# Performance work log

Measured on AMD Instinct MI355X. Metric: run time of the kernel, lower is better.

Reference implementation:

```python
import jax, jax.numpy as jnp
import numpy as np

N = 100000
E = 500000
HID = 256
N_EDGE_TYPES = 5
N_ATOM = 16
N_CHARGE = 7
NUM_RBF = 16
CUTOFF = 5.0
LN_EPS = 1e-5


def _xavier(key, shape):
    fan_in, fan_out = shape[0], shape[1]
    lim = float(np.sqrt(6.0 / (fan_in + fan_out)))
    return jax.random.uniform(key, shape, jnp.float32, -lim, lim)


def setup_inputs() -> dict:
    key = jax.random.key(0)
    ks = jax.random.split(key, 12)
    input_dim = HID * 2 + NUM_RBF + N_ATOM + N_CHARGE  # 551
    h = jax.random.normal(ks[0], (N, HID), jnp.float32)
    x = jax.random.normal(ks[1], (N, 3), jnp.float32)
    spawn_node_idx = jax.random.randint(ks[2], (E,), 0, N)
    existing_node_idx = jax.random.randint(ks[3], (E,), 0, N)
    ins_x = jax.random.normal(ks[4], (E, 3), jnp.float32)
    ins_a = jax.random.randint(ks[5], (E,), 0, N_ATOM)
    ins_c = jax.random.randint(ks[6], (E,), 0, N_CHARGE)
    # MLP params (Xavier weights, zero biases; LayerNorm gamma=1, beta=0)
    W1 = _xavier(ks[7], (input_dim, HID)); b1 = jnp.zeros((HID,), jnp.float32)
    g1 = jnp.ones((HID,), jnp.float32); be1 = jnp.zeros((HID,), jnp.float32)
    W2 = _xavier(ks[8], (HID, HID // 2)); b2 = jnp.zeros((HID // 2,), jnp.float32)
    g2 = jnp.ones((HID // 2,), jnp.float32); be2 = jnp.zeros((HID // 2,), jnp.float32)
    W3 = _xavier(ks[9], (HID // 2, N_EDGE_TYPES)); b3 = jnp.zeros((N_EDGE_TYPES,), jnp.float32)
    # Gaussian RBF parameters: centers on [0, cutoff], shared width from spacing
    rbf_mu = jnp.linspace(0.0, CUTOFF, NUM_RBF).astype(jnp.float32)
    delta = CUTOFF / (NUM_RBF - 1)
    rbf_gamma = jnp.asarray(1.0 / (2.0 * delta * delta), jnp.float32)
    return {"h": h, "x": x, "spawn_node_idx": spawn_node_idx,
            "existing_node_idx": existing_node_idx, "ins_x": ins_x,
            "ins_a": ins_a, "ins_c": ins_c,
            "W1": W1, "b1": b1, "g1": g1, "be1": be1,
            "W2": W2, "b2": b2, "g2": g2, "be2": be2,
            "W3": W3, "b3": b3, "rbf_mu": rbf_mu, "rbf_gamma": rbf_gamma}


def _layer_norm(z, gamma, beta):
    mu = jnp.mean(z, axis=-1, keepdims=True)
    var = jnp.mean((z - mu) ** 2, axis=-1, keepdims=True)
    return (z - mu) * jax.lax.rsqrt(var + LN_EPS) * gamma + beta


def reference(h, x, spawn_node_idx, existing_node_idx, ins_x, ins_a, ins_c,
              W1, b1, g1, be1, W2, b2, g2, be2, W3, b3, rbf_mu, rbf_gamma):
    # gather node pairs  [E, HID] / [E, 3]
    h_spawn = h[spawn_node_idx]
    h_existing = h[existing_node_idx]
    existing_pos = x[existing_node_idx]
    # distance + Gaussian RBF  [E, NUM_RBF]
    d = jnp.maximum(jnp.linalg.norm(ins_x - existing_pos, axis=-1), 1e-6)
    dist_features = jnp.exp(-rbf_gamma * (d[:, None] - rbf_mu) ** 2)
    # one-hot insertion type features
    ins_atom = jax.nn.one_hot(ins_a, N_ATOM, dtype=h.dtype)
    ins_charge = jax.nn.one_hot(ins_c, N_CHARGE, dtype=h.dtype)
    feats = jnp.concatenate([h_spawn, h_existing, dist_features, ins_atom, ins_charge], axis=-1)
    # 3-layer MLP: Linear -> LN -> SiLU -> Linear -> LN -> SiLU -> Linear
    z = jax.nn.silu(_layer_norm(feats @ W1 + b1, g1, be1))
    z = jax.nn.silu(_layer_norm(z @ W2 + b2, g2, be2))
    return z @ W3 + b3  # [E, N_EDGE_TYPES]
```

## Files before the change

kernel.cpp:

```cpp
#include <hip/hip_runtime.h>
#include <stdint.h>

#define NN 100000
#define EE 500000
#define HIDD 256
#define LN_EPS 1e-5f

typedef _Float16 half8 __attribute__((ext_vector_type(8)));
typedef _Float16 half4 __attribute__((ext_vector_type(4)));
typedef __fp16 fp16x2 __attribute__((ext_vector_type(2)));
typedef float f32x4 __attribute__((ext_vector_type(4)));
typedef float f32x2 __attribute__((ext_vector_type(2)));

#define LBAR() asm volatile("s_waitcnt lgkmcnt(0)\n\ts_barrier" ::: "memory")

__device__ __forceinline__ unsigned short f2h(float f) {
  _Float16 h = (_Float16)f;
  union { _Float16 hh; unsigned short us; } u; u.hh = h;
  return u.us;
}

__device__ __forceinline__ unsigned pkrtz(float a, float b) {
  union { fp16x2 h; unsigned u; } c;
  c.h = __builtin_amdgcn_cvt_pkrtz(a, b);
  return c.u;
}

__device__ __forceinline__ float fast_silu(float y) {
  float e = __expf(-y);
  return y * __builtin_amdgcn_rcpf(1.f + e);
}

__device__ __forceinline__ half8 ldg8(const unsigned short* p) {
  return *(const half8*)p;
}

__device__ __forceinline__ int4 cvt_row(const float* s) {
  float4 a0 = *(const float4*)s, a1 = *(const float4*)(s + 4);
  uint4 ua;
  ua.x = pkrtz(a0.x, a0.y); ua.y = pkrtz(a0.z, a0.w);
  ua.z = pkrtz(a1.x, a1.y); ua.w = pkrtz(a1.z, a1.w);
  return *(int4*)&ua;
}

__global__ __launch_bounds__(256) void prep_kern(const float* __restrict__ h,
                                                 const float* __restrict__ W1,
                                                 const float* __restrict__ W2,
                                                 const float* __restrict__ W3,
                                                 unsigned short* __restrict__ hb,
                                                 unsigned short* __restrict__ w1sw,
                                                 unsigned short* __restrict__ w2sw,
                                                 unsigned short* __restrict__ w3sw) {
  int b = blockIdx.x;
  if (b < 712) {
    int t = b * 256 + threadIdx.x;
    if (t < 147456) {
      int chunk = t >> 14, rem = t & 16383;
      int kq = rem >> 11, n = (rem >> 3) & 255, j = rem & 7;
      int k = (chunk << 6) + (kq << 3) + j;
      float v = (k < 551) ? W1[k * 256 + n] : 0.f;
      w1sw[t] = f2h(v);
    } else if (t < 147456 + 32768) {
      int t2 = t - 147456;
      int chunk = t2 >> 13, rem = t2 & 8191;
      int kq = rem >> 10, n = (rem >> 3) & 127, j = rem & 7;
      int k = (chunk << 6) + (kq << 3) + j;
      w2sw[t2] = f2h(W2[k * 128 + n]);
    } else if (t < 147456 + 32768 + 2048) {
      int t3 = t - 180224;
      int kq = t3 >> 7, o = (t3 >> 3) & 15, j = t3 & 7;
      int k = (kq << 3) + j;
      w3sw[t3] = f2h((o < 5) ? W3[k * 5 + o] : 0.f);
    }
  } else {
    int i = ((b - 712) * 256 + threadIdx.x) * 8;
    float4 v0 = *(const float4*)(h + i);
    float4 v1 = *(const float4*)(h + i + 4);
    uint4 u;
    u.x = pkrtz(v0.x, v0.y); u.y = pkrtz(v0.z, v0.w);
    u.z = pkrtz(v1.x, v1.y); u.w = pkrtz(v1.z, v1.w);
    *(uint4*)(hb + i) = u;
  }
}

struct __align__(16) SMem {
  short r1[16384];
  float red[512];
  _Float16 b1h[256], g1h[256], be1h[256];
  _Float16 b2h[128], g2h[128], be2h[128];
  float muv[16];
  float b3v[8];
  int spI[64], exI[64];
};

__global__ __launch_bounds__(256, 3)
void edge_head_main(const float* __restrict__ h, const float* __restrict__ x,
                    const int* __restrict__ spawn, const int* __restrict__ exist,
                    const float* __restrict__ insx, const int* __restrict__ insa,
                    const int* __restrict__ insc,
                    const float* __restrict__ b1, const float* __restrict__ g1,
                    const float* __restrict__ be1,
                    const float* __restrict__ b2, const float* __restrict__ g2,
                    const float* __restrict__ be2,
                    const float* __restrict__ b3, const float* __restrict__ mu,
                    const float* __restrict__ gammaP,
                    const unsigned short* __restrict__ w1sw,
                    const unsigned short* __restrict__ w2sw,
                    const unsigned short* __restrict__ w3swg,
                    const unsigned short* __restrict__ hb, int use_hb,
                    float* __restrict__ out) {
  __shared__ SMem sm;
  const int t = threadIdx.x;
  const int base = blockIdx.x * 64;
  const int lane = t & 63;
  const int wv = t >> 6;
  const int cl = lane & 15;
  const int q = lane >> 4;
  const int sx = (cl & 7) << 3;

  sm.b1h[t] = (_Float16)b1[t]; sm.g1h[t] = (_Float16)g1[t]; sm.be1h[t] = (_Float16)be1[t];
  if (t < 128) { sm.b2h[t] = (_Float16)b2[t]; sm.g2h[t] = (_Float16)g2[t]; sm.be2h[t] = (_Float16)be2[t]; }
  if (t < 16) sm.muv[t] = mu[t];
  if (t < 8) sm.b3v[t] = (t < 5) ? b3[t] : 0.f;
  if (t < 64) {
    int e = base + t; int ec = e < EE ? e : EE - 1;
    sm.spI[t] = spawn[ec]; sm.exI[t] = exist[ec];
  }
  const float gma = gammaP[0];

  LBAR();

  float dreg = 0.f;
  int k1 = 16, k2 = 32;
  if (t < 64) {
    int e = base + t; int ec = e < EE ? e : EE - 1;
    float ix0 = insx[ec * 3], ix1 = insx[ec * 3 + 1], ix2 = insx[ec * 3 + 2];
    int nd = sm.exI[t];
    float dx = ix0 - x[nd * 3], dy = ix1 - x[nd * 3 + 1], dz = ix2 - x[nd * 3 + 2];
    dreg = fmaxf(sqrtf(dx * dx + dy * dy + dz * dz), 1e-6f);
    k1 = 16 + insa[ec]; k2 = 32 + insc[ec];
  }

  const int row0 = t >> 3, p0 = t & 7;
  const int row1 = row0 + 32;
  const int sw0 = ((p0 ^ (row0 & 7)) << 3);
  const int sw1 = ((p0 ^ (row1 & 7)) << 3);

  const size_t oSp0 = (size_t)sm.spI[row0] * HIDD + p0 * 8;
  const size_t oSp1 = (size_t)sm.spI[row1] * HIDD + p0 * 8;
  const size_t oEx0 = (size_t)sm.exI[row0] * HIDD + p0 * 8;
  const size_t oEx1 = (size_t)sm.exI[row1] * HIDD + p0 * 8;
  const char* bSp0 = use_hb ? (const char*)(hb + oSp0) : (const char*)(h + oSp0);
  const char* bSp1 = use_hb ? (const char*)(hb + oSp1) : (const char*)(h + oSp1);
  const char* bEx0 = use_hb ? (const char*)(hb + oEx0) : (const char*)(h + oEx0);
  const char* bEx1 = use_hb ? (const char*)(hb + oEx1) : (const char*)(h + oEx1);

#define GLOAD(lc, PA, PB) do {                                          \
    const int g_ = (lc) - 1;                                            \
    const int colb_ = (g_ & 3) * 64;                                    \
    const char* b0_ = (g_ < 4) ? bSp0 : bEx0;                           \
    const char* b1_ = (g_ < 4) ? bSp1 : bEx1;                           \
    if (use_hb) {                                                       \
      PA = *(const int4*)(b0_ + colb_ * 2);                             \
      PB = *(const int4*)(b1_ + colb_ * 2);                             \
    } else {                                                            \
      PA = cvt_row((const float*)(b0_ + colb_ * 4));                    \
      PB = cvt_row((const float*)(b1_ + colb_ * 4));                    \
    }                                                                   \
  } while (0)

  int4 pA1, pB1, pA0, pB0;
  GLOAD(1, pA1, pB1);
  GLOAD(2, pA0, pB0);

  const unsigned short* w1p = w1sw + q * 2048 + wv * 512 + cl * 8;
  half8 fA[4], fB[4];
#pragma unroll
  for (int i = 0; i < 4; ++i) fA[i] = ldg8(w1p + 8 * 16384 + i * 128);
#pragma unroll
  for (int i = 0; i < 4; ++i) fB[i] = ldg8(w1p + 8 * 16384 + 8192 + i * 128);

  if (t < 64) {
    short* rp = &sm.r1[t * 64];
    const int sw = t & 7;
    float rb[16];
#pragma unroll
    for (int k = 0; k < 16; ++k) { float dd = dreg - sm.muv[k]; rb[k] = __expf(-gma * dd * dd); }
    uint4 ua, ub;
    ua.x = pkrtz(rb[0], rb[1]);  ua.y = pkrtz(rb[2], rb[3]);
    ua.z = pkrtz(rb[4], rb[5]);  ua.w = pkrtz(rb[6], rb[7]);
    ub.x = pkrtz(rb[8], rb[9]);  ub.y = pkrtz(rb[10], rb[11]);
    ub.z = pkrtz(rb[12], rb[13]); ub.w = pkrtz(rb[14], rb[15]);
    *(int4*)&rp[(0 ^ sw) * 8] = *(int4*)&ua;
    *(int4*)&rp[(1 ^ sw) * 8] = *(int4*)&ub;
    const int4 z4 = {0, 0, 0, 0};
#pragma unroll
    for (int g = 2; g < 8; ++g) *(int4*)&rp[(g ^ sw) * 8] = z4;
    rp[((k1 >> 3) ^ sw) * 8 + (k1 & 7)] = (short)0x3C00;
    rp[((k2 >> 3) ^ sw) * 8 + (k2 & 7)] = (short)0x3C00;
  }

  LBAR();

  f32x4 acc[4][4];
#pragma unroll
  for (int i = 0; i < 4; ++i)
#pragma unroll
    for (int j = 0; j < 4; ++j) acc[i][j] = (f32x4){0.f, 0.f, 0.f, 0.f};

#pragma unroll
  for (int c = 0; c < 9; ++c) {
    if (c < 8) {
      const int nb = ((c + 1) & 1) * 4096;
      if ((c & 1) == 0) {
        *(int4*)&sm.r1[nb + row0 * 64 + sw0] = pA1;
        *(int4*)&sm.r1[nb + row1 * 64 + sw1] = pB1;
        if (c <= 5) GLOAD(c + 3, pA1, pB1);
      } else {
        *(int4*)&sm.r1[nb + row0 * 64 + sw0] = pA0;
        *(int4*)&sm.r1[nb + row1 * 64 + sw1] = pB0;
        if (c <= 5) GLOAD(c + 3, pA0, pB0);
      }
    }
    const int cb = (c & 1) * 4096;
    {
      half8 bf[4];
#pragma unroll
      for (int j = 0; j < 4; ++j)
        bf[j] = *(const half8*)&sm.r1[cb + (j * 16 + cl) * 64 + ((q * 8) ^ sx)];
#pragma unroll
      for (int i = 0; i < 4; ++i)
#pragma unroll
        for (int j = 0; j < 4; ++j)
          acc[i][j] = __builtin_amdgcn_mfma_f32_16x16x32_f16(fA[i], bf[j], acc[i][j], 0, 0, 0);
    }
    if (c < 8) {
      const unsigned short* wp = w1p + c * 16384;
#pragma unroll
      for (int i = 0; i < 4; ++i) fA[i] = ldg8(wp + i * 128);
    }
    {
      half8 bf[4];
#pragma unroll
      for (int j = 0; j < 4; ++j)
        bf[j] = *(const half8*)&sm.r1[cb + (j * 16 + cl) * 64 + ((32 + q * 8) ^ sx)];
#pragma unroll
      for (int i = 0; i < 4; ++i)
#pragma unroll
        for (int j = 0; j < 4; ++j)
          acc[i][j] = __builtin_amdgcn_mfma_f32_16x16x32_f16(fB[i], bf[j], acc[i][j], 0, 0, 0);
    }
    if (c < 8) {
      const unsigned short* wp = w1p + c * 16384 + 8192;
#pragma unroll
      for (int i = 0; i < 4; ++i) fB[i] = ldg8(wp + i * 128);
    }
    LBAR();
  }
#undef GLOAD

  f32x2 bb1[4][2];
#pragma unroll
  for (int i = 0; i < 4; ++i) {
    half4 b4 = *(const half4*)&sm.b1h[wv * 64 + i * 16 + q * 4];
    bb1[i][0] = (f32x2){(float)b4[0], (float)b4[1]};
    bb1[i][1] = (f32x2){(float)b4[2], (float)b4[3]};
  }
  float S1arr[4], Q1arr[4];
#pragma unroll
  for (int j = 0; j < 4; ++j) {
    f32x2 S2 = (f32x2){0.f, 0.f}, Q2 = (f32x2){0.f, 0.f};
#pragma unroll
    for (int i = 0; i < 4; ++i) {
      f32x2 v0 = (f32x2){acc[i][j][0], acc[i][j][1]} + bb1[i][0];
      f32x2 v1 = (f32x2){acc[i][j][2], acc[i][j][3]} + bb1[i][1];
      acc[i][j][0] = v0[0]; acc[i][j][1] = v0[1];
      acc[i][j][2] = v1[0]; acc[i][j][3] = v1[1];
      S2 += v0 + v1;
      Q2 += v0 * v0;
      Q2 += v1 * v1;
    }
    float S = S2[0] + S2[1], Q = Q2[0] + Q2[1];
    S += __shfl_xor(S, 16); S += __shfl_xor(S, 32);
    Q += __shfl_xor(Q, 16); Q += __shfl_xor(Q, 32);
    S1arr[j] = S; Q1arr[j] = Q;
  }
  if (q == 0) {
#pragma unroll
    for (int j = 0; j < 4; ++j) {
      sm.red[wv * 64 + j * 16 + cl] = S1arr[j];
      sm.red[256 + wv * 64 + j * 16 + cl] = Q1arr[j];
    }
  }
  LBAR();
  f32x2 rs1[4], mr1[4];
#pragma unroll
  for (int j = 0; j < 4; ++j) {
    int m = j * 16 + cl;
    float S = sm.red[m] + sm.red[64 + m] + sm.red[128 + m] + sm.red[192 + m];
    float Q = sm.red[256 + m] + sm.red[320 + m] + sm.red[384 + m] + sm.red[448 + m];
    float mn = S * (1.f / 256.f);
    float rs = rsqrtf(Q * (1.f / 256.f) - mn * mn + LN_EPS);
    rs1[j] = (f32x2){rs, rs};
    mr1[j] = (f32x2){-mn * rs, -mn * rs};
  }
#pragma unroll
  for (int i = 0; i < 4; ++i) {
    half4 g4 = *(const half4*)&sm.g1h[wv * 64 + i * 16 + q * 4];
    half4 e4 = *(const half4*)&sm.be1h[wv * 64 + i * 16 + q * 4];
    f32x2 gg0 = (f32x2){(float)g4[0], (float)g4[1]}, gg1 = (f32x2){(float)g4[2], (float)g4[3]};
    f32x2 ee0 = (f32x2){(float)e4[0], (float)e4[1]}, ee1 = (f32x2){(float)e4[2], (float)e4[3]};
#pragma unroll
    for (int j = 0; j < 4; ++j) {
      f32x2 v0 = (f32x2){acc[i][j][0], acc[i][j][1]};
      f32x2 v1 = (f32x2){acc[i][j][2], acc[i][j][3]};
      f32x2 t0 = v0 * rs1[j] + mr1[j];
      f32x2 t1 = v1 * rs1[j] + mr1[j];
      f32x2 y0 = t0 * gg0 + ee0;
      f32x2 y1 = t1 * gg1 + ee1;
      float s0 = fast_silu(y0[0]), s1 = fast_silu(y0[1]);
      float s2 = fast_silu(y1[0]), s3 = fast_silu(y1[1]);
      uint2 w; w.x = pkrtz(s0, s1); w.y = pkrtz(s2, s3);
      int m = j * 16 + cl;
      int k0 = wv * 64 + i * 16 + q * 4;
      *(uint2*)&sm.r1[m * 256 + (k0 ^ ((m & 7) << 3))] = w;
    }
  }
  LBAR();

  half8 af3[4];
#pragma unroll
  for (int ks = 0; ks < 4; ++ks)
    af3[ks] = ldg8(w3swg + (ks * 4 + q) * 128 + cl * 8);

  const unsigned short* w2p = w2sw + q * 1024 + wv * 256 + cl * 8;
  f32x4 acc2[2][4];
#pragma unroll
  for (int i = 0; i < 2; ++i)
#pragma unroll
    for (int j = 0; j < 4; ++j) acc2[i][j] = (f32x4){0.f, 0.f, 0.f, 0.f};
#pragma unroll
  for (int c2 = 0; c2 < 4; ++c2) {
#pragma unroll
    for (int ks = 0; ks < 2; ++ks) {
      half8 a0 = ldg8(w2p + c2 * 8192 + ks * 4096);
      half8 a1 = ldg8(w2p + c2 * 8192 + ks * 4096 + 128);
      half8 bf[4];
#pragma unroll
      for (int j = 0; j < 4; ++j)
        bf[j] = *(const half8*)&sm.r1[(j * 16 + cl) * 256 + ((c2 * 64 + ks * 32 + q * 8) ^ sx)];
#pragma unroll
      for (int j = 0; j < 4; ++j) {
        acc2[0][j] = __builtin_amdgcn_mfma_f32_16x16x32_f16(a0, bf[j], acc2[0][j], 0, 0, 0);
        acc2[1][j] = __builtin_amdgcn_mfma_f32_16x16x32_f16(a1, bf[j], acc2[1][j], 0, 0, 0);
      }
    }
  }

  f32x2 bb2[2][2];
#pragma unroll
  for (int i = 0; i < 2; ++i) {
    half4 b4 = *(const half4*)&sm.b2h[wv * 32 + i * 16 + q * 4];
    bb2[i][0] = (f32x2){(float)b4[0], (float)b4[1]};
    bb2[i][1] = (f32x2){(float)b4[2], (float)b4[3]};
  }
  float S2arr[4], Q2arr[4];
#pragma unroll
  for (int j = 0; j < 4; ++j) {
    f32x2 S2 = (f32x2){0.f, 0.f}, Q2 = (f32x2){0.f, 0.f};
#pragma unroll
    for (int i = 0; i < 2; ++i) {
      f32x2 v0 = (f32x2){acc2[i][j][0], acc2[i][j][1]} + bb2[i][0];
      f32x2 v1 = (f32x2){acc2[i][j][2], acc2[i][j][3]} + bb2[i][1];
      acc2[i][j][0] = v0[0]; acc2[i][j][1] = v0[1];
      acc2[i][j][2] = v1[0]; acc2[i][j][3] = v1[1];
      S2 += v0 + v1;
      Q2 += v0 * v0;
      Q2 += v1 * v1;
    }
    float S = S2[0] + S2[1], Q = Q2[0] + Q2[1];
    S += __shfl_xor(S, 16); S += __shfl_xor(S, 32);
    Q += __shfl_xor(Q, 16); Q += __shfl_xor(Q, 32);
    S2arr[j] = S; Q2arr[j] = Q;
  }
  if (q == 0) {
#pragma unroll
    for (int j = 0; j < 4; ++j) {
      sm.red[wv * 64 + j * 16 + cl] = S2arr[j];
      sm.red[256 + wv * 64 + j * 16 + cl] = Q2arr[j];
    }
  }
  LBAR();
  f32x2 rs2[4], mr2[4];
#pragma unroll
  for (int j = 0; j < 4; ++j) {
    int m = j * 16 + cl;
    float S = sm.red[m] + sm.red[64 + m] + sm.red[128 + m] + sm.red[192 + m];
    float Q = sm.red[256 + m] + sm.red[320 + m] + sm.red[384 + m] + sm.red[448 + m];
    float mn = S * (1.f / 128.f);
    float rs = rsqrtf(Q * (1.f / 128.f) - mn * mn + LN_EPS);
    rs2[j] = (f32x2){rs, rs};
    mr2[j] = (f32x2){-mn * rs, -mn * rs};
  }
#pragma unroll
  for (int i = 0; i < 2; ++i) {
    half4 g4 = *(const half4*)&sm.g2h[wv * 32 + i * 16 + q * 4];
    half4 e4 = *(const half4*)&sm.be2h[wv * 32 + i * 16 + q * 4];
    f32x2 gg0 = (f32x2){(float)g4[0], (float)g4[1]}, gg1 = (f32x2){(float)g4[2], (float)g4[3]};
    f32x2 ee0 = (f32x2){(float)e4[0], (float)e4[1]}, ee1 = (f32x2){(float)e4[2], (float)e4[3]};
#pragma unroll
    for (int j = 0; j < 4; ++j) {
      f32x2 v0 = (f32x2){acc2[i][j][0], acc2[i][j][1]};
      f32x2 v1 = (f32x2){acc2[i][j][2], acc2[i][j][3]};
      f32x2 t0 = v0 * rs2[j] + mr2[j];
      f32x2 t1 = v1 * rs2[j] + mr2[j];
      f32x2 y0 = t0 * gg0 + ee0;
      f32x2 y1 = t1 * gg1 + ee1;
      float s0 = fast_silu(y0[0]), s1 = fast_silu(y0[1]);
      float s2 = fast_silu(y1[0]), s3 = fast_silu(y1[1]);
      uint2 w; w.x = pkrtz(s0, s1); w.y = pkrtz(s2, s3);
      int m = j * 16 + cl;
      int k0 = wv * 32 + i * 16 + q * 4;
      *(uint2*)&sm.r1[m * 128 + (k0 ^ ((m & 7) << 3))] = w;
    }
  }
  LBAR();

  f32x4 a3 = (f32x4){0.f, 0.f, 0.f, 0.f};
  const int m3 = wv * 16 + cl;
  const int sx3 = (m3 & 7) << 3;
#pragma unroll
  for (int ks = 0; ks < 4; ++ks) {
    half8 bfv = *(const half8*)&sm.r1[m3 * 128 + ((ks * 32 + q * 8) ^ sx3)];
    a3 = __builtin_amdgcn_mfma_f32_16x16x32_f16(af3[ks], bfv, a3, 0, 0, 0);
  }
#pragma unroll
  for (int r = 0; r < 4; ++r) {
    int o = q * 4 + r;
    if (o < 5) sm.red[m3 * 5 + o] = a3[r] + sm.b3v[o];
  }
  LBAR();
  if (t < 80) {
    size_t g = (size_t)base * 5 + (size_t)t * 4;
    if (g + 4 <= (size_t)EE * 5) {
      *(float4*)(out + g) = *(const float4*)&sm.red[t * 4];
    } else {
#pragma unroll
      for (int u = 0; u < 4; ++u)
        if (g + u < (size_t)EE * 5) out[g + u] = sm.red[t * 4 + u];
    }
  }
}

extern "C" void kernel_launch(void* const* d_in, const int* in_sizes, int n_in,
                              void* d_out, int out_size, void* d_ws, size_t ws_size,
                              hipStream_t stream) {
  const float* h    = (const float*)d_in[0];
  const float* x    = (const float*)d_in[1];
  const int* spawn  = (const int*)d_in[2];
  const int* exist  = (const int*)d_in[3];
  const float* insx = (const float*)d_in[4];
  const int* insa   = (const int*)d_in[5];
  const int* insc   = (const int*)d_in[6];
  const float* W1   = (const float*)d_in[7];
  const float* b1   = (const float*)d_in[8];
  const float* g1   = (const float*)d_in[9];
  const float* be1  = (const float*)d_in[10];
  const float* W2   = (const float*)d_in[11];
  const float* b2   = (const float*)d_in[12];
  const float* g2   = (const float*)d_in[13];
  const float* be2  = (const float*)d_in[14];
  const float* W3   = (const float*)d_in[15];
  const float* b3   = (const float*)d_in[16];
  const float* mu   = (const float*)d_in[17];
  const float* gma  = (const float*)d_in[18];

  unsigned short* w1sw = (unsigned short*)d_ws;
  unsigned short* w2sw = w1sw + 147456;
  unsigned short* w3sw = w2sw + 32768;
  unsigned short* hb   = w3sw + 2048;
  const size_t need_hb = 364544ull + (size_t)NN * HIDD * 2ull;
  int use_hb = (ws_size >= need_hb) ? 1 : 0;

  prep_kern<<<use_hb ? 13212 : 712, 256, 0, stream>>>(h, W1, W2, W3, hb, w1sw, w2sw, w3sw);
  edge_head_main<<<7813, 256, 0, stream>>>(h, x, spawn, exist, insx, insa, insc,
                                           b1, g1, be1, b2, g2, be2, b3, mu, gma,
                                           w1sw, w2sw, w3sw, hb, use_hb,
                                           (float*)d_out);
}
```

Baseline: 419.6 us.

## Stage gathered rows in 128-column chunks with fewer barriers and separate feature buffer

Restructures the first-layer GEMM pipeline. Each barrier phase now stages two 64-column chunks of gathered node features in LDS (four loads per thread) instead of one, which halves the number of barriers. The RBF/one-hot features move to their own LDS buffer and are processed after the main loop. W1 fragments are no longer prefetched a step ahead; they are loaded right before use. The cost is more LDS per block, which may lower occupancy from the 3-blocks target, and possibly more exposed global latency on the weight loads.

```diff
diff --git a/kernel.cpp b/kernel.cpp
--- a/kernel.cpp
+++ b/kernel.cpp
@@ -85,6 +85,7 @@
 
 struct __align__(16) SMem {
   short r1[16384];
+  short feats[4096];
   float red[512];
   _Float16 b1h[256], g1h[256], be1h[256];
   _Float16 b2h[128], g2h[128], be2h[128];
@@ -155,33 +156,35 @@
   const char* bEx0 = use_hb ? (const char*)(hb + oEx0) : (const char*)(h + oEx0);
   const char* bEx1 = use_hb ? (const char*)(hb + oEx1) : (const char*)(h + oEx1);
 
-#define GLOAD(lc, PA, PB) do {                                          \
-    const int g_ = (lc) - 1;                                            \
-    const int colb_ = (g_ & 3) * 64;                                    \
-    const char* b0_ = (g_ < 4) ? bSp0 : bEx0;                           \
-    const char* b1_ = (g_ < 4) ? bSp1 : bEx1;                           \
+  int4 pS0, pS1, pS2, pS3;
+#define GLOAD2(ph) do {                                                 \
+    const char* b0_ = ((ph) < 2) ? bSp0 : bEx0;                         \
+    const char* b1_ = ((ph) < 2) ? bSp1 : bEx1;                         \
+    const int ce_ = ((ph) & 1) * 128;             \
     if (use_hb) {                                                       \
-      PA = *(const int4*)(b0_ + colb_ * 2);                             \
-      PB = *(const int4*)(b1_ + colb_ * 2);                             \
+      pS0 = *(const int4*)(b0_ + ce_ * 2);                              \
+      pS1 = *(const int4*)(b1_ + ce_ * 2);                              \
+      pS2 = *(const int4*)(b0_ + (ce_ + 64) * 2);                       \
+      pS3 = *(const int4*)(b1_ + (ce_ + 64) * 2);                       \
     } else {                                                            \
-      PA = cvt_row((const float*)(b0_ + colb_ * 4));                    \
-      PB = cvt_row((const float*)(b1_ + colb_ * 4));                    \
+      pS0 = cvt_row((const float*)(b0_ + ce_ * 4));                     \
+      pS1 = cvt_row((const float*)(b1_ + ce_ * 4));                     \
+      pS2 = cvt_row((const float*)(b0_ + (ce_ + 64) * 4));              \
+      pS3 = cvt_row((const float*)(b1_ + (ce_ + 64) * 4));              \
     }                                                                   \
   } while (0)
 
-  int4 pA1, pB1, pA0, pB0;
-  GLOAD(1, pA1, pB1);
-  GLOAD(2, pA0, pB0);
+  GLOAD2(0);
+  *(int4*)&sm.r1[row0 * 64 + sw0] = pS0;
+  *(int4*)&sm.r1[row1 * 64 + sw1] = pS1;
+  *(int4*)&sm.r1[4096 + row0 * 64 + sw0] = pS2;
+  *(int4*)&sm.r1[4096 + row1 * 64 + sw1] = pS3;
+  GLOAD2(1);
 
   const unsigned short* w1p = w1sw + q * 2048 + wv * 512 + cl * 8;
-  half8 fA[4], fB[4];
-#pragma unroll
-  for (int i = 0; i < 4; ++i) fA[i] = ldg8(w1p + 8 * 16384 + i * 128);
-#pragma unroll
-  for (int i = 0; i < 4; ++i) fB[i] = ldg8(w1p + 8 * 16384 + 8192 + i * 128);
 
   if (t < 64) {
-    short* rp = &sm.r1[t * 64];
+    short* rp = &sm.feats[t * 64];
     const int sw = t & 7;
     float rb[16];
 #pragma unroll
@@ -209,55 +212,55 @@
     for (int j = 0; j < 4; ++j) acc[i][j] = (f32x4){0.f, 0.f, 0.f, 0.f};
 
 #pragma unroll
-  for (int c = 0; c < 9; ++c) {
-    if (c < 8) {
-      const int nb = ((c + 1) & 1) * 4096;
-      if ((c & 1) == 0) {
-        *(int4*)&sm.r1[nb + row0 * 64 + sw0] = pA1;
-        *(int4*)&sm.r1[nb + row1 * 64 + sw1] = pB1;
-        if (c <= 5) GLOAD(c + 3, pA1, pB1);
-      } else {
-        *(int4*)&sm.r1[nb + row0 * 64 + sw0] = pA0;
-        *(int4*)&sm.r1[nb + row1 * 64 + sw1] = pB0;
-        if (c <= 5) GLOAD(c + 3, pA0, pB0);
+  for (int p = 0; p < 4; ++p) {
+    if (p < 3) {
+      const int nb = ((p + 1) & 1) * 8192;
+      *(int4*)&sm.r1[nb + row0 * 64 + sw0] = pS0;
+      *(int4*)&sm.r1[nb + row1 * 64 + sw1] = pS1;
+      *(int4*)&sm.r1[nb + 4096 + row0 * 64 + sw0] = pS2;
+      *(int4*)&sm.r1[nb + 4096 + row1 * 64 + sw1] = pS3;
+      if (p < 2) GLOAD2(p + 2);
+    }
+    const int cb = (p & 1) * 8192;
+#pragma unroll
+    for (int ch = 0; ch < 2; ++ch) {
+      const unsigned short* wp = w1p + (2 * p + ch) * 16384;
+#pragma unroll
+      for (int ks = 0; ks < 2; ++ks) {
+        half8 bf[4], fX[4];
+#pragma unroll
+        for (int j = 0; j < 4; ++j)
+          bf[j] = *(const half8*)&sm.r1[cb + ch * 4096 + (j * 16 + cl) * 64 + ((ks * 32 + q * 8) ^ sx)];
+#pragma unroll
+        for (int i = 0; i < 4; ++i) fX[i] = ldg8(wp + ks * 8192 + i * 128);
+#pragma unroll
+        for (int i = 0; i < 4; ++i)
+#pragma unroll
+          for (int j = 0; j < 4; ++j)
+            acc[i][j] = __builtin_amdgcn_mfma_f32_16x16x32_f16(fX[i], bf[j], acc[i][j], 0, 0, 0);
       }
     }
-    const int cb = (c & 1) * 4096;
-    {
-      half8 bf[4];
+    if (p < 3) LBAR();
+  }
+#undef GLOAD2
+
+  {
+    const unsigned short* wp = w1p + 8 * 16384;
+#pragma unroll
+    for (int ks = 0; ks < 2; ++ks) {
+      half8 bf[4], fX[4];
 #pragma unroll
       for (int j = 0; j < 4; ++j)
-        bf[j] = *(const half8*)&sm.r1[cb + (j * 16 + cl) * 64 + ((q * 8) ^ sx)];
+        bf[j] = *(const half8*)&sm.feats[(j * 16 + cl) * 64 + ((ks * 32 + q * 8) ^ sx)];
+#pragma unroll
+      for (int i = 0; i < 4; ++i) fX[i] = ldg8(wp + ks * 8192 + i * 128);
 #pragma unroll
       for (int i = 0; i < 4; ++i)
 #pragma unroll
         for (int j = 0; j < 4; ++j)
-          acc[i][j] = __builtin_amdgcn_mfma_f32_16x16x32_f16(fA[i], bf[j], acc[i][j], 0, 0, 0);
-    }
-    if (c < 8) {
-      const unsigned short* wp = w1p + c * 16384;
-#pragma unroll
-      for (int i = 0; i < 4; ++i) fA[i] = ldg8(wp + i * 128);
-    }
-    {
-      half8 bf[4];
-#pragma unroll
-      for (int j = 0; j < 4; ++j)
-        bf[j] = *(const half8*)&sm.r1[cb + (j * 16 + cl) * 64 + ((32 + q * 8) ^ sx)];
-#pragma unroll
-      for (int i = 0; i < 4; ++i)
-#pragma unroll
-        for (int j = 0; j < 4; ++j)
-          acc[i][j] = __builtin_amdgcn_mfma_f32_16x16x32_f16(fB[i], bf[j], acc[i][j], 0, 0, 0);
-    }
-    if (c < 8) {
-      const unsigned short* wp = w1p + c * 16384 + 8192;
-#pragma unroll
-      for (int i = 0; i < 4; ++i) fB[i] = ldg8(wp + i * 128);
-    }
-    LBAR();
-  }
-#undef GLOAD
+          acc[i][j] = __builtin_amdgcn_mfma_f32_16x16x32_f16(fX[i], bf[j], acc[i][j], 0, 0, 0);
+    }
+  }
 
   f32x2 bb1[4][2];
 #pragma unroll
```

Result: no change. 421.8 us (+0.5%).
